# Kernel tuning notes

Measured on AMD Instinct MI355X. Metric: run time of the kernel, lower is better.

Reference implementation:

```python
import jax, jax.numpy as jnp
import numpy as np

CPS = 16          # coarse_patch_size = 128 / resolution[0](=8)
ENC = 128         # enc_dim = CPS*CPS/2
LN_EPS = 1e-5


def setup_inputs() -> dict:
    key = jax.random.key(0)
    ks = jax.random.split(key, 10)
    B, C, H, W = 4, 256, 160, 160
    s = 0.05
    return {
        "feat_c1": jax.random.normal(ks[0], (B, C, H, W), dtype=jnp.float32),
        "feat_c2": jax.random.normal(ks[1], (B, C, H, W), dtype=jnp.float32),
        "mask_c1": jnp.ones((1, H, W), dtype=bool),
        "img_conv_w": jax.random.normal(ks[2], (1, C), dtype=jnp.float32) * s,
        "img_conv_b": jnp.zeros((1,), jnp.float32),
        "img_w1": jax.random.normal(ks[3], (2 * ENC, 2 * ENC), dtype=jnp.float32) * s,
        "img_w2": jax.random.normal(ks[4], (ENC, 2 * ENC), dtype=jnp.float32) * s,
        "img_ln_g": jnp.ones((ENC,), jnp.float32),
        "img_ln_b": jnp.zeros((ENC,), jnp.float32),
        "depth_conv_w": jax.random.normal(ks[5], (1, C), dtype=jnp.float32) * s,
        "depth_conv_b": jnp.zeros((1,), jnp.float32),
        "depth_w1": jax.random.normal(ks[6], (2 * ENC, 2 * ENC), dtype=jnp.float32) * s,
        "depth_w2": jax.random.normal(ks[7], (ENC, 2 * ENC), dtype=jnp.float32) * s,
        "depth_ln_g": jnp.ones((ENC,), jnp.float32),
        "depth_ln_b": jnp.zeros((ENC,), jnp.float32),
        "logit_scale": jnp.asarray(np.log(1.0 / 0.07), jnp.float32),
    }


def _grid_from_mask(mask_c1):
    # replicate get_patches: grid size from max lit row/col of the mask
    m = np.asarray(mask_c1)[0]
    inds = np.argwhere(m)
    feat_h = int(inds[:, 0].max()) + 1
    feat_w = int(inds[:, 1].max()) + 1
    nv = int(feat_w / CPS + 0.5)   # outer loop count (row starts), as in source
    nh = int(feat_h / CPS + 0.5)   # inner loop count (col starts)
    return nv, nh


def _extract_patches(feat, nv, nh):
    # vectorized equivalent of the nested python-loop gather: non-overlapping
    # CPS x CPS tiles, row-major order matching (r outer, c inner)
    B, C = feat.shape[0], feat.shape[1]
    f = feat[:, :, : nv * CPS, : nh * CPS]
    f = f.reshape(B, C, nv, CPS, nh, CPS)
    f = f.transpose(0, 2, 4, 1, 3, 5)          # [B, nv, nh, C, CPS, CPS]
    return f.reshape(B * nv * nh, C, CPS, CPS)


def _branch(patches, conv_w, conv_b, w1, w2, ln_g, ln_b):
    # conv1x1 (256 -> 1) + ReLU
    x = jnp.einsum("bchw,oc->bohw", patches, conv_w) + conv_b[None, :, None, None]
    x = jax.nn.relu(x)
    x = x.reshape(x.shape[0], -1)              # [B*N, 2*ENC]
    # Linear(no bias) -> ReLU -> Linear(no bias)
    x = jax.nn.relu(x @ w1.T) @ w2.T           # [B*N, ENC]
    mu = jnp.mean(x, axis=-1, keepdims=True)
    var = jnp.var(x, axis=-1, keepdims=True)
    return (x - mu) / jnp.sqrt(var + LN_EPS) * ln_g + ln_b


def reference(feat_c1, feat_c2, mask_c1, img_conv_w, img_conv_b, img_w1, img_w2,
              img_ln_g, img_ln_b, depth_conv_w, depth_conv_b, depth_w1, depth_w2,
              depth_ln_g, depth_ln_b, logit_scale):
    nv, nh = _grid_from_mask(mask_c1)
    N = nv * nh
    B = feat_c1.shape[0]
    p1 = _extract_patches(feat_c1, nv, nh)
    p2 = _extract_patches(feat_c2, nv, nh)
    e1 = _branch(p1, img_conv_w, img_conv_b, img_w1, img_w2, img_ln_g, img_ln_b)
    e2 = _branch(p2, depth_conv_w, depth_conv_b, depth_w1, depth_w2, depth_ln_g, depth_ln_b)
    e1 = e1.reshape(B, N, ENC)
    e2 = e2.reshape(B, N, ENC)
    scale = jnp.exp(logit_scale)
    logits_per_img = scale * jnp.einsum("bnd,bmd->bnm", e1, e2)   # [B, N, N]
    logits_per_depth = jnp.swapaxes(logits_per_img, 1, 2)
    return logits_per_img, logits_per_depth
```

## Files before the change

### kernel.cpp

```cpp
#include <hip/hip_runtime.h>
#include <math.h>

#define CPS 16
#define ENC 128
#define NH 10
#define NPATCH 100
#define BATCH 4
#define CCH 256
#define WIDTH 160
#define HW 25600
#define ROWS_TOTAL 400
#define CSPLIT 8
#define CHPG 32

typedef float vf4 __attribute__((ext_vector_type(4)));

__global__ __launch_bounds__(256, 4) void conv_partial_kernel(
    const float* __restrict__ f1, const float* __restrict__ f2,
    const float* __restrict__ wci, const float* __restrict__ wcd,
    float* __restrict__ partial)
{
    int lane = threadIdx.x & 63;
    int wv   = threadIdx.x >> 6;

    int bid   = blockIdx.x;
    int plane = bid & 7;
    int split = (bid >> 3) & 7;
    int chunk = bid >> 6;
    int branch = plane >> 2;
    int b      = plane & 3;

    const float* f    = branch ? f2  : f1;
    const float* wsel = (branch ? wcd : wci) + split * CHPG;

    int px = chunk * 1024 + wv * 256 + lane * 4;
    const float* fb = f + ((size_t)(b * CCH + split * CHPG)) * HW + px;

    vf4 acc = (vf4)(0.f);
    #pragma unroll
    for (int h = 0; h < 2; ++h) {
        vf4 v[16];
        #pragma unroll
        for (int j = 0; j < 16; ++j)
            v[j] = __builtin_nontemporal_load(
                       (const vf4*)(fb + (size_t)(h * 16 + j) * HW));
        #pragma unroll
        for (int j = 0; j < 16; ++j) {
            float wc = wsel[h * 16 + j];
            acc += v[j] * wc;
        }
    }

    *(vf4*)(partial + ((size_t)(split * 8 + plane)) * HW + px) = acc;
}

__global__ __launch_bounds__(256) void mlp_ln_kernel(
    const float* __restrict__ partial,
    const float* __restrict__ bci,  const float* __restrict__ bcd,
    const float* __restrict__ w1i, const float* __restrict__ w2i,
    const float* __restrict__ gi,  const float* __restrict__ bli,
    const float* __restrict__ w1d, const float* __restrict__ w2d,
    const float* __restrict__ gd,  const float* __restrict__ bld,
    float* __restrict__ e)
{
    const int R = 4;
    __shared__ float xs[R][256];
    __shared__ float ys[R][256];
    __shared__ float zs[R][ENC];

    int tid    = threadIdx.x;
    int branch = blockIdx.x / 100;
    int row0   = (blockIdx.x % 100) * R;

    const float* w1 = branch ? w1d : w1i;
    const float* w2 = branch ? w2d : w2i;
    const float* g  = branch ? gd  : gi;
    const float* bl = branch ? bld : bli;
    float bias      = branch ? bcd[0] : bci[0];

    {
        int hh = tid >> 4, ww = tid & 15;
        #pragma unroll
        for (int r = 0; r < R; ++r) {
            int prow  = row0 + r;
            int b     = prow / 100;
            int patch = prow % 100;
            int pv = patch / 10, ph = patch % 10;
            int pixel = (pv * 16 + hh) * WIDTH + ph * 16 + ww;
            int plane = branch * BATCH + b;
            float v = bias;
            #pragma unroll
            for (int s = 0; s < CSPLIT; ++s)
                v += partial[((size_t)(s * 8 + plane)) * HW + pixel];
            xs[r][tid] = fmaxf(v, 0.f);
        }
    }
    __syncthreads();

    {
        float acc[R] = {0.f, 0.f, 0.f, 0.f};
        const float4* w1r = (const float4*)(w1 + (size_t)tid * 256);
        #pragma unroll 4
        for (int c4 = 0; c4 < 64; ++c4) {
            float4 wv = w1r[c4];
            #pragma unroll
            for (int r = 0; r < R; ++r) {
                float4 xv = *(const float4*)(&xs[r][c4 * 4]);
                acc[r] = fmaf(xv.x, wv.x, acc[r]);
                acc[r] = fmaf(xv.y, wv.y, acc[r]);
                acc[r] = fmaf(xv.z, wv.z, acc[r]);
                acc[r] = fmaf(xv.w, wv.w, acc[r]);
            }
        }
        #pragma unroll
        for (int r = 0; r < R; ++r) ys[r][tid] = fmaxf(acc[r], 0.f);
    }
    __syncthreads();

    #pragma unroll
    for (int i = 0; i < 2; ++i) {
        int idx = tid + 256 * i;
        int r = idx >> 7, m = idx & 127;
        float acc = 0.f;
        const float4* w2r = (const float4*)(w2 + (size_t)m * 256);
        #pragma unroll 4
        for (int c4 = 0; c4 < 64; ++c4) {
            float4 wv = w2r[c4];
            float4 yv = *(const float4*)(&ys[r][c4 * 4]);
            acc = fmaf(yv.x, wv.x, acc);
            acc = fmaf(yv.y, wv.y, acc);
            acc = fmaf(yv.z, wv.z, acc);
            acc = fmaf(yv.w, wv.w, acc);
        }
        zs[r][m] = acc;
    }
    __syncthreads();

    int r = tid >> 6, lane = tid & 63;
    float a  = zs[r][lane];
    float b2 = zs[r][lane + 64];
    float s = a + b2;
    float q = a * a + b2 * b2;
    #pragma unroll
    for (int off = 32; off >= 1; off >>= 1) {
        s += __shfl_xor(s, off);
        q += __shfl_xor(q, off);
    }
    float mu  = s * (1.f / 128.f);
    float var = q * (1.f / 128.f) - mu * mu;
    float inv = 1.f / sqrtf(var + 1e-5f);
    float* erow = e + ((size_t)(branch * ROWS_TOTAL + row0 + r)) * ENC;
    erow[lane]      = (a  - mu) * inv * g[lane]      + bl[lane];
    erow[lane + 64] = (b2 - mu) * inv * g[lane + 64] + bl[lane + 64];
}

__global__ __launch_bounds__(256) void logits_kernel(
    const float* __restrict__ e, const float* __restrict__ lsc,
    float* __restrict__ out)
{
    int gidx = blockIdx.x * 256 + threadIdx.x;
    if (gidx >= BATCH * NPATCH * NPATCH) return;
    float scale = expf(lsc[0]);

    int b    = gidx / (NPATCH * NPATCH);
    int rrem = gidx % (NPATCH * NPATCH);
    int n = rrem / NPATCH, m = rrem % NPATCH;

    const float4* e1 = (const float4*)(e + (size_t)(b * NPATCH + n) * ENC);
    const float4* e2 = (const float4*)(e + (size_t)(ROWS_TOTAL + b * NPATCH + m) * ENC);
    float acc = 0.f;
    #pragma unroll 8
    for (int c4 = 0; c4 < ENC / 4; ++c4) {
        float4 av = e1[c4], bv = e2[c4];
        acc = fmaf(av.x, bv.x, acc);
        acc = fmaf(av.y, bv.y, acc);
        acc = fmaf(av.z, bv.z, acc);
        acc = fmaf(av.w, bv.w, acc);
    }
    float L = scale * acc;
    out[gidx] = L;
    out[BATCH * NPATCH * NPATCH + b * NPATCH * NPATCH + m * NPATCH + n] = L;
}

extern "C" void kernel_launch(void* const* d_in, const int* in_sizes, int n_in,
                              void* d_out, int out_size, void* d_ws, size_t ws_size,
                              hipStream_t stream) {
    const float* f1  = (const float*)d_in[0];
    const float* f2  = (const float*)d_in[1];
    const float* wci = (const float*)d_in[3];
    const float* bci = (const float*)d_in[4];
    const float* w1i = (const float*)d_in[5];
    const float* w2i = (const float*)d_in[6];
    const float* gi  = (const float*)d_in[7];
    const float* bli = (const float*)d_in[8];
    const float* wcd = (const float*)d_in[9];
    const float* bcd = (const float*)d_in[10];
    const float* w1d = (const float*)d_in[11];
    const float* w2d = (const float*)d_in[12];
    const float* gd  = (const float*)d_in[13];
    const float* bld = (const float*)d_in[14];
    const float* lsc = (const float*)d_in[15];

    float* partial = (float*)d_ws;
    float* e       = partial + CSPLIT * 8 * HW;
    float* out = (float*)d_out;

    conv_partial_kernel<<<1600, 256, 0, stream>>>(f1, f2, wci, wcd, partial);
    mlp_ln_kernel<<<200, 256, 0, stream>>>(partial, bci, bcd,
                                           w1i, w2i, gi, bli,
                                           w1d, w2d, gd, bld, e);
    logits_kernel<<<(BATCH * NPATCH * NPATCH + 255) / 256, 256, 0, stream>>>(e, lsc, out);
}
```

Measured before the change: 268.5 us.

## Fuse 1x1 conv reduction with MLP and LayerNorm into one per-patch-pair kernel

The conv channel reduction is merged into the MLP/LayerNorm kernel. Each 512-thread block handles two horizontally adjacent patches, splitting the channels across 8 waves and reducing them in shared memory, so the partial-sum workspace round trip and one launch go away. The cost is only 400 blocks streaming the ~105 MB of features. Loads are plain rather than nontemporal, 32-float row segments give shorter contiguous accesses, and the MLP weights are re-read per block, which may lower achieved bandwidth.

```diff
diff --git a/kernel.cpp b/kernel.cpp
--- a/kernel.cpp
+++ b/kernel.cpp
@@ -3,155 +3,138 @@
 
 #define CPS 16
 #define ENC 128
-#define NH 10
 #define NPATCH 100
 #define BATCH 4
 #define CCH 256
 #define WIDTH 160
 #define HW 25600
 #define ROWS_TOTAL 400
-#define CSPLIT 8
-#define CHPG 32
 
 typedef float vf4 __attribute__((ext_vector_type(4)));
 
-__global__ __launch_bounds__(256, 4) void conv_partial_kernel(
+__global__ __launch_bounds__(512, 4) void fused_branch_kernel(
     const float* __restrict__ f1, const float* __restrict__ f2,
-    const float* __restrict__ wci, const float* __restrict__ wcd,
-    float* __restrict__ partial)
-{
-    int lane = threadIdx.x & 63;
-    int wv   = threadIdx.x >> 6;
-
-    int bid   = blockIdx.x;
-    int plane = bid & 7;
-    int split = (bid >> 3) & 7;
-    int chunk = bid >> 6;
-    int branch = plane >> 2;
-    int b      = plane & 3;
-
-    const float* f    = branch ? f2  : f1;
-    const float* wsel = (branch ? wcd : wci) + split * CHPG;
-
-    int px = chunk * 1024 + wv * 256 + lane * 4;
-    const float* fb = f + ((size_t)(b * CCH + split * CHPG)) * HW + px;
-
-    vf4 acc = (vf4)(0.f);
-    #pragma unroll
-    for (int h = 0; h < 2; ++h) {
-        vf4 v[16];
-        #pragma unroll
-        for (int j = 0; j < 16; ++j)
-            v[j] = __builtin_nontemporal_load(
-                       (const vf4*)(fb + (size_t)(h * 16 + j) * HW));
-        #pragma unroll
-        for (int j = 0; j < 16; ++j) {
-            float wc = wsel[h * 16 + j];
-            acc += v[j] * wc;
-        }
-    }
-
-    *(vf4*)(partial + ((size_t)(split * 8 + plane)) * HW + px) = acc;
-}
-
-__global__ __launch_bounds__(256) void mlp_ln_kernel(
-    const float* __restrict__ partial,
-    const float* __restrict__ bci,  const float* __restrict__ bcd,
+    const float* __restrict__ wci, const float* __restrict__ bci,
     const float* __restrict__ w1i, const float* __restrict__ w2i,
     const float* __restrict__ gi,  const float* __restrict__ bli,
+    const float* __restrict__ wcd, const float* __restrict__ bcd,
     const float* __restrict__ w1d, const float* __restrict__ w2d,
     const float* __restrict__ gd,  const float* __restrict__ bld,
     float* __restrict__ e)
 {
-    const int R = 4;
-    __shared__ float xs[R][256];
-    __shared__ float ys[R][256];
-    __shared__ float zs[R][ENC];
+    __shared__ float xs_part[8][512];
+    __shared__ float xs[2][256];
+    __shared__ float ys[2][256];
+    __shared__ float zs2[2][2][128];
 
-    int tid    = threadIdx.x;
-    int branch = blockIdx.x / 100;
-    int row0   = (blockIdx.x % 100) * R;
+    int tid  = threadIdx.x;
+    int lane = tid & 63;
+    int wv   = tid >> 6;
 
+    int bid    = blockIdx.x;
+    int branch = bid / 200;
+    int rem    = bid % 200;
+    int pp     = rem % 5;
+    int bpv    = rem / 5;
+    int b      = bpv / 10;
+    int pv     = bpv % 10;
+
+    const float* f  = branch ? f2  : f1;
+    const float* wc = branch ? wcd : wci;
     const float* w1 = branch ? w1d : w1i;
     const float* w2 = branch ? w2d : w2i;
     const float* g  = branch ? gd  : gi;
     const float* bl = branch ? bld : bli;
     float bias      = branch ? bcd[0] : bci[0];
 
+    int rowA = lane >> 3;
+    int col4 = (lane & 7) * 4;
+    const float* fb = f + ((size_t)(b * CCH + wv * 32)) * HW
+                        + (size_t)(pv * CPS + rowA) * WIDTH + pp * 32 + col4;
+    vf4 accA = (vf4)(0.f), accB = (vf4)(0.f);
+    #pragma unroll
+    for (int h = 0; h < 4; ++h) {
+        vf4 va[8], vb[8];
+        #pragma unroll
+        for (int j = 0; j < 8; ++j) {
+            const float* p0 = fb + (size_t)(h * 8 + j) * HW;
+            va[j] = *(const vf4*)p0;
+            vb[j] = *(const vf4*)(p0 + 8 * WIDTH);
+        }
+        #pragma unroll
+        for (int j = 0; j < 8; ++j) {
+            float w = wc[wv * 32 + h * 8 + j];
+            accA += va[j] * w;
+            accB += vb[j] * w;
+        }
+    }
+    *(vf4*)&xs_part[wv][rowA * 32 + col4]       = accA;
+    *(vf4*)&xs_part[wv][(rowA + 8) * 32 + col4] = accB;
+    __syncthreads();
+
     {
-        int hh = tid >> 4, ww = tid & 15;
+        float v = bias;
         #pragma unroll
-        for (int r = 0; r < R; ++r) {
-            int prow  = row0 + r;
-            int b     = prow / 100;
-            int patch = prow % 100;
-            int pv = patch / 10, ph = patch % 10;
-            int pixel = (pv * 16 + hh) * WIDTH + ph * 16 + ww;
-            int plane = branch * BATCH + b;
-            float v = bias;
-            #pragma unroll
-            for (int s = 0; s < CSPLIT; ++s)
-                v += partial[((size_t)(s * 8 + plane)) * HW + pixel];
-            xs[r][tid] = fmaxf(v, 0.f);
-        }
+        for (int s = 0; s < 8; ++s) v += xs_part[s][tid];
+        int rr = tid >> 5, colS = tid & 31;
+        xs[colS >> 4][rr * 16 + (colS & 15)] = fmaxf(v, 0.f);
     }
     __syncthreads();
 
     {
-        float acc[R] = {0.f, 0.f, 0.f, 0.f};
-        const float4* w1r = (const float4*)(w1 + (size_t)tid * 256);
+        int o = tid & 255, p = tid >> 8;
+        const float4* w1r = (const float4*)(w1 + (size_t)o * 256);
+        float acc = 0.f;
         #pragma unroll 4
         for (int c4 = 0; c4 < 64; ++c4) {
-            float4 wv = w1r[c4];
-            #pragma unroll
-            for (int r = 0; r < R; ++r) {
-                float4 xv = *(const float4*)(&xs[r][c4 * 4]);
-                acc[r] = fmaf(xv.x, wv.x, acc[r]);
-                acc[r] = fmaf(xv.y, wv.y, acc[r]);
-                acc[r] = fmaf(xv.z, wv.z, acc[r]);
-                acc[r] = fmaf(xv.w, wv.w, acc[r]);
-            }
+            float4 wv4 = w1r[c4];
+            float4 xv  = *(const float4*)&xs[p][c4 * 4];
+            acc = fmaf(xv.x, wv4.x, acc);
+            acc = fmaf(xv.y, wv4.y, acc);
+            acc = fmaf(xv.z, wv4.z, acc);
+            acc = fmaf(xv.w, wv4.w, acc);
         }
-        #pragma unroll
-        for (int r = 0; r < R; ++r) ys[r][tid] = fmaxf(acc[r], 0.f);
+        ys[p][o] = fmaxf(acc, 0.f);
     }
     __syncthreads();
 
-    #pragma unroll
-    for (int i = 0; i < 2; ++i) {
-        int idx = tid + 256 * i;
-        int r = idx >> 7, m = idx & 127;
+    {
+        int m = tid & 127, p = (tid >> 7) & 1, half = tid >> 8;
+        const float4* w2r = (const float4*)(w2 + (size_t)m * 256);
         float acc = 0.f;
-        const float4* w2r = (const float4*)(w2 + (size_t)m * 256);
         #pragma unroll 4
-        for (int c4 = 0; c4 < 64; ++c4) {
-            float4 wv = w2r[c4];
-            float4 yv = *(const float4*)(&ys[r][c4 * 4]);
-            acc = fmaf(yv.x, wv.x, acc);
-            acc = fmaf(yv.y, wv.y, acc);
-            acc = fmaf(yv.z, wv.z, acc);
-            acc = fmaf(yv.w, wv.w, acc);
+        for (int i = 0; i < 32; ++i) {
+            int c4 = half * 32 + i;
+            float4 wv4 = w2r[c4];
+            float4 yv  = *(const float4*)&ys[p][c4 * 4];
+            acc = fmaf(yv.x, wv4.x, acc);
+            acc = fmaf(yv.y, wv4.y, acc);
+            acc = fmaf(yv.z, wv4.z, acc);
+            acc = fmaf(yv.w, wv4.w, acc);
         }
-        zs[r][m] = acc;
+        zs2[half][p][m] = acc;
     }
     __syncthreads();
 
-    int r = tid >> 6, lane = tid & 63;
-    float a  = zs[r][lane];
-    float b2 = zs[r][lane + 64];
-    float s = a + b2;
-    float q = a * a + b2 * b2;
-    #pragma unroll
-    for (int off = 32; off >= 1; off >>= 1) {
-        s += __shfl_xor(s, off);
-        q += __shfl_xor(q, off);
+    if (tid < 128) {
+        int p = tid >> 6;
+        float a  = zs2[0][p][lane]      + zs2[1][p][lane];
+        float b2 = zs2[0][p][lane + 64] + zs2[1][p][lane + 64];
+        float s = a + b2;
+        float q = a * a + b2 * b2;
+        #pragma unroll
+        for (int off = 32; off >= 1; off >>= 1) {
+            s += __shfl_xor(s, off);
+            q += __shfl_xor(q, off);
+        }
+        float mu  = s * (1.f / 128.f);
+        float var = q * (1.f / 128.f) - mu * mu;
+        float inv = 1.f / sqrtf(var + 1e-5f);
+        int prow = b * NPATCH + pv * 10 + pp * 2 + p;
+        float* erow = e + ((size_t)(branch * ROWS_TOTAL + prow)) * ENC;
+        erow[lane]      = (a  - mu) * inv * g[lane]      + bl[lane];
+        erow[lane + 64] = (b2 - mu) * inv * g[lane + 64] + bl[lane + 64];
     }
-    float mu  = s * (1.f / 128.f);
-    float var = q * (1.f / 128.f) - mu * mu;
-    float inv = 1.f / sqrtf(var + 1e-5f);
-    float* erow = e + ((size_t)(branch * ROWS_TOTAL + row0 + r)) * ENC;
-    erow[lane]      = (a  - mu) * inv * g[lane]      + bl[lane];
-    erow[lane + 64] = (b2 - mu) * inv * g[lane + 64] + bl[lane + 64];
 }
 
 __global__ __launch_bounds__(256) void logits_kernel(
@@ -201,13 +184,11 @@
     const float* bld = (const float*)d_in[14];
     const float* lsc = (const float*)d_in[15];
 
-    float* partial = (float*)d_ws;
-    float* e       = partial + CSPLIT * 8 * HW;
+    float* e   = (float*)d_ws;
     float* out = (float*)d_out;
 
-    conv_partial_kernel<<<1600, 256, 0, stream>>>(f1, f2, wci, wcd, partial);
-    mlp_ln_kernel<<<200, 256, 0, stream>>>(partial, bci, bcd,
-                                           w1i, w2i, gi, bli,
-                                           w1d, w2d, gd, bld, e);
+    fused_branch_kernel<<<400, 512, 0, stream>>>(f1, f2,
+                                                 wci, bci, w1i, w2i, gi, bli,
+                                                 wcd, bcd, w1d, w2d, gd, bld, e);
     logits_kernel<<<(BATCH * NPATCH * NPATCH + 255) / 256, 256, 0, stream>>>(e, lsc, out);
 }
```

Measured after the change: 297.1 us. +10.7%, slower.
